# Optimization experiments

Measured on AMD Instinct MI355X. Metric: run time of the kernel, lower is better.

## Reference

```python
import jax, jax.numpy as jnp
import numpy as np

LENGTH_SCALE = 0.1


def setup_inputs() -> dict:
    key = jax.random.key(0)
    k1, k2, k3 = jax.random.split(key, 3)
    features = jax.random.normal(k1, (8, 512, 128, 128), dtype=jnp.float32)
    # nn.Parameter init: normal(0, 0.05)
    weights = jax.random.normal(k2, (16, 64, 512), dtype=jnp.float32) * 0.05
    m = jax.random.normal(k3, (16, 64), dtype=jnp.float32)
    N = jnp.ones((64,), dtype=jnp.float32) * 12.0  # buffer init: ones * 12
    return {"features": features, "weights": weights, "m": m, "N": N}


def reference(features, weights, m, N):
    # per-class linear embedding projection: [b,f,h,w] x [e,c,f] -> [b,e,c,h,w]
    embeddings = jnp.einsum('bfhw,ecf->bechw', features, weights)
    centroids = m / N  # [e, c]
    gamma = -1.0 / (2.0 * LENGTH_SCALE ** 2)
    diff = embeddings - centroids[None, :, :, None, None]
    # squared L2, mean over embedding dim e, RBF exp -> [b, c, h, w]
    out = jnp.exp(jnp.mean(diff * diff, axis=1) * gamma)
    return out
```

## Files before the change

### kernel.cpp

```cpp
#include <hip/hip_runtime.h>

typedef __attribute__((ext_vector_type(8))) short bf16x8;
typedef __attribute__((ext_vector_type(4))) float f32x4;
typedef __attribute__((ext_vector_type(4))) float f4;
typedef __attribute__((ext_vector_type(2))) unsigned int u32x2;
typedef __attribute__((ext_vector_type(4))) unsigned int u32x4;

#define HW   16384
#define FDIM 512

__device__ __forceinline__ unsigned pkhi(float a, float b) {
    return __builtin_amdgcn_perm(__builtin_bit_cast(unsigned int, b),
                                 __builtin_bit_cast(unsigned int, a),
                                 0x07060302u);
}
__device__ __forceinline__ float trhi(float a) {
    return __builtin_bit_cast(float, __builtin_bit_cast(unsigned int, a) & 0xFFFF0000u);
}
__device__ __forceinline__ unsigned pklo(float a, float b) {
    return pkhi(a - trhi(a), b - trhi(b));
}

__global__ __launch_bounds__(256) void duq_fused(
    const float* __restrict__ feat,
    const float* __restrict__ wts,
    const float* __restrict__ m_in,
    const float* __restrict__ n_in,
    float* __restrict__ out)
{
    __shared__ __align__(16) unsigned short Ah[128 * 40];
    __shared__ __align__(16) unsigned short Al[128 * 40];
    __shared__ __align__(16) unsigned short Bh[128 * 40];
    __shared__ __align__(16) unsigned short Bl[128 * 40];

    const int t  = threadIdx.x;
    const int bx = blockIdx.x;
    const int nb = bx & 7;
    const int mb = bx >> 3;
    const int bidx = mb >> 7;
    const int hw0  = (mb & 127) << 7;

    const int fb = t & 7;
    const int pb = t >> 3;
    const float* ap = feat + (size_t)bidx * (FDIM * HW) + (size_t)(fb * 4) * HW + (hw0 + pb * 4);

    const int bn  = t >> 1;
    const int bh_ = t & 1;
    const int ng  = nb * 128 + bn;
    const float* bp = wts + (size_t)((ng & 15) * 64 + (ng >> 4)) * FDIM + bh_ * 16;

    unsigned short* awH = &Ah[(pb * 4) * 40 + fb * 4];
    unsigned short* awL = &Al[(pb * 4) * 40 + fb * 4];
    unsigned short* bwH = &Bh[bn * 40 + bh_ * 16];
    unsigned short* bwL = &Bl[bn * 40 + bh_ * 16];

    const int lane = t & 63;
    const int wv = t >> 6;
    const int wm = wv >> 1, wn = wv & 1;
    const int l16 = lane & 15, qd = lane >> 4;

    const unsigned short* arH = &Ah[(wm * 64 + l16) * 40 + qd * 8];
    const unsigned short* arL = &Al[(wm * 64 + l16) * 40 + qd * 8];
    const unsigned short* brH = &Bh[(wn * 64 + l16) * 40 + qd * 8];
    const unsigned short* brL = &Bl[(wn * 64 + l16) * 40 + qd * 8];

    f32x4 acc[4][4] = {};

    f4 av[4], bv[4];
    #pragma unroll
    for (int i = 0; i < 4; ++i) av[i] = *(const f4*)(ap + (size_t)i * HW);
    #pragma unroll
    for (int q = 0; q < 4; ++q) bv[q] = *(const f4*)(bp + q * 4);

    for (int kt = 0; kt < 16; ++kt) {
        __syncthreads();
        #pragma unroll
        for (int j = 0; j < 4; ++j) {
            float a0 = av[0][j], a1 = av[1][j], a2 = av[2][j], a3 = av[3][j];
            u32x2 h, l;
            h[0] = pkhi(a0, a1); h[1] = pkhi(a2, a3);
            l[0] = pklo(a0, a1); l[1] = pklo(a2, a3);
            *(u32x2*)(awH + j * 40) = h;
            *(u32x2*)(awL + j * 40) = l;
        }
        {
            u32x4 h0 = { pkhi(bv[0][0], bv[0][1]), pkhi(bv[0][2], bv[0][3]),
                         pkhi(bv[1][0], bv[1][1]), pkhi(bv[1][2], bv[1][3]) };
            u32x4 h1 = { pkhi(bv[2][0], bv[2][1]), pkhi(bv[2][2], bv[2][3]),
                         pkhi(bv[3][0], bv[3][1]), pkhi(bv[3][2], bv[3][3]) };
            u32x4 l0 = { pklo(bv[0][0], bv[0][1]), pklo(bv[0][2], bv[0][3]),
                         pklo(bv[1][0], bv[1][1]), pklo(bv[1][2], bv[1][3]) };
            u32x4 l1 = { pklo(bv[2][0], bv[2][1]), pklo(bv[2][2], bv[2][3]),
                         pklo(bv[3][0], bv[3][1]), pklo(bv[3][2], bv[3][3]) };
            *(u32x4*)(bwH)     = h0;  *(u32x4*)(bwH + 8) = h1;
            *(u32x4*)(bwL)     = l0;  *(u32x4*)(bwL + 8) = l1;
        }
        __syncthreads();

        if (kt < 15) {
            ap += 32 * HW;
            bp += 32;
            #pragma unroll
            for (int i = 0; i < 4; ++i) av[i] = *(const f4*)(ap + (size_t)i * HW);
            #pragma unroll
            for (int q = 0; q < 4; ++q) bv[q] = *(const f4*)(bp + q * 4);
        }

        bf16x8 fah[4], fal[4];
        #pragma unroll
        for (int i = 0; i < 4; ++i) {
            fah[i] = *(const bf16x8*)(arH + i * 640);
            fal[i] = *(const bf16x8*)(arL + i * 640);
        }
        #pragma unroll
        for (int j = 0; j < 4; ++j) {
            bf16x8 fbh = *(const bf16x8*)(brH + j * 640);
            bf16x8 fbl = *(const bf16x8*)(brL + j * 640);
            #pragma unroll
            for (int i = 0; i < 4; ++i) {
                acc[i][j] = __builtin_amdgcn_mfma_f32_16x16x32_bf16(fah[i], fbh, acc[i][j], 0, 0, 0);
                acc[i][j] = __builtin_amdgcn_mfma_f32_16x16x32_bf16(fah[i], fbl, acc[i][j], 0, 0, 0);
                acc[i][j] = __builtin_amdgcn_mfma_f32_16x16x32_bf16(fal[i], fbh, acc[i][j], 0, 0, 0);
            }
        }
    }

    float centv[4];
    #pragma unroll
    for (int j = 0; j < 4; ++j) {
        int cj = nb * 8 + wn * 4 + j;
        centv[j] = m_in[l16 * 64 + cj] / n_in[cj];
    }
    #pragma unroll
    for (int i = 0; i < 4; ++i) {
        #pragma unroll
        for (int j = 0; j < 4; ++j) {
            float s0 = acc[i][j][0] - centv[j]; s0 *= s0;
            float s1 = acc[i][j][1] - centv[j]; s1 *= s1;
            float s2 = acc[i][j][2] - centv[j]; s2 *= s2;
            float s3 = acc[i][j][3] - centv[j]; s3 *= s3;
            #pragma unroll
            for (int msk = 1; msk < 16; msk <<= 1) {
                s0 += __shfl_xor(s0, msk, 64);
                s1 += __shfl_xor(s1, msk, 64);
                s2 += __shfl_xor(s2, msk, 64);
                s3 += __shfl_xor(s3, msk, 64);
            }
            if (l16 == 0) {
                int cj = nb * 8 + wn * 4 + j;
                f4 o;
                o[0] = __expf(s0 * -3.125f);
                o[1] = __expf(s1 * -3.125f);
                o[2] = __expf(s2 * -3.125f);
                o[3] = __expf(s3 * -3.125f);
                size_t off = ((size_t)(bidx * 64 + cj)) * HW
                           + (size_t)(hw0 + wm * 64 + i * 16 + qd * 4);
                *(f4*)(out + off) = o;
            }
        }
    }
}

extern "C" void kernel_launch(void* const* d_in, const int* in_sizes, int n_in,
                              void* d_out, int out_size, void* d_ws, size_t ws_size,
                              hipStream_t stream) {
    const float* feat = (const float*)d_in[0];
    const float* wts  = (const float*)d_in[1];
    const float* mbuf = (const float*)d_in[2];
    const float* nbuf = (const float*)d_in[3];
    float* out = (float*)d_out;
    duq_fused<<<dim3(1024 * 8), dim3(256), 0, stream>>>(feat, wts, mbuf, nbuf, out);
}
```

Measured before the change: 754.8 us.

## Precompute bf16 hi/lo weight split in prepass and stream B fragments from global

Adds a small pre-kernel that converts the weights once per call into bf16 hi/lo arrays in workspace, laid out in MFMA fragment order. The main kernel then drops the B shared-memory tiles and per-block weight conversion, loading B fragments straight from global (L2) with one-step register prefetch. It also sets launch_bounds occupancy to 4 blocks. This removes redundant conversion work and LDS traffic, at the cost of an extra launch, more global/L2 loads per wave, and a fallback path when workspace is too small.

```diff
diff --git a/kernel.cpp b/kernel.cpp
--- a/kernel.cpp
+++ b/kernel.cpp
@@ -21,11 +21,147 @@
     return pkhi(a - trhi(a), b - trhi(b));
 }
 
-__global__ __launch_bounds__(256) void duq_fused(
+__global__ __launch_bounds__(256) void conv_w(const float* __restrict__ wts,
+                                              unsigned short* __restrict__ wh,
+                                              unsigned short* __restrict__ wl) {
+    const int tid = blockIdx.x * 256 + threadIdx.x;
+    const int n  = tid & 1023;
+    const int kc = tid >> 10;
+    const float* src = wts + (size_t)((n & 15) * 64 + (n >> 4)) * FDIM + kc * 8;
+    f4 a = *(const f4*)src, b = *(const f4*)(src + 4);
+    u32x4 h = { pkhi(a[0], a[1]), pkhi(a[2], a[3]), pkhi(b[0], b[1]), pkhi(b[2], b[3]) };
+    u32x4 l = { pklo(a[0], a[1]), pklo(a[2], a[3]), pklo(b[0], b[1]), pklo(b[2], b[3]) };
+    size_t off = ((size_t)kc * 1024 + n) * 8;
+    *(u32x4*)(wh + off) = h;
+    *(u32x4*)(wl + off) = l;
+}
+
+__global__ __launch_bounds__(256, 4) void duq_main(
     const float* __restrict__ feat,
-    const float* __restrict__ wts,
+    const unsigned short* __restrict__ wh,
+    const unsigned short* __restrict__ wl,
     const float* __restrict__ m_in,
     const float* __restrict__ n_in,
+    float* __restrict__ out)
+{
+    __shared__ __align__(16) unsigned short Ah[128 * 40];
+    __shared__ __align__(16) unsigned short Al[128 * 40];
+
+    const int t  = threadIdx.x;
+    const int bx = blockIdx.x;
+    const int nb = bx & 7;
+    const int mb = bx >> 3;
+    const int bidx = mb >> 7;
+    const int hw0  = (mb & 127) << 7;
+
+    const int fb = t & 7;
+    const int pb = t >> 3;
+    const float* ap = feat + (size_t)bidx * (FDIM * HW) + (size_t)(fb * 4) * HW + (hw0 + pb * 4);
+    unsigned short* awH = &Ah[(pb * 4) * 40 + fb * 4];
+    unsigned short* awL = &Al[(pb * 4) * 40 + fb * 4];
+
+    const int lane = t & 63;
+    const int wv = t >> 6;
+    const int wm = wv >> 1, wn = wv & 1;
+    const int l16 = lane & 15, qd = lane >> 4;
+
+    const unsigned short* arH = &Ah[(wm * 64 + l16) * 40 + qd * 8];
+    const unsigned short* arL = &Al[(wm * 64 + l16) * 40 + qd * 8];
+
+    const size_t bgoff = ((size_t)qd * 1024 + (size_t)(nb * 128 + wn * 64 + l16)) * 8;
+    const unsigned short* bgh = wh + bgoff;
+    const unsigned short* bgl = wl + bgoff;
+
+    f32x4 acc[4][4] = {};
+
+    f4 av[4];
+    #pragma unroll
+    for (int i = 0; i < 4; ++i) av[i] = *(const f4*)(ap + (size_t)i * HW);
+
+    bf16x8 cbh = *(const bf16x8*)(bgh);
+    bf16x8 cbl = *(const bf16x8*)(bgl);
+    size_t boff = 0;
+
+    for (int kt = 0; kt < 16; ++kt) {
+        __syncthreads();
+        #pragma unroll
+        for (int j = 0; j < 4; ++j) {
+            float a0 = av[0][j], a1 = av[1][j], a2 = av[2][j], a3 = av[3][j];
+            u32x2 h, l;
+            h[0] = pkhi(a0, a1); h[1] = pkhi(a2, a3);
+            l[0] = pklo(a0, a1); l[1] = pklo(a2, a3);
+            *(u32x2*)(awH + j * 40) = h;
+            *(u32x2*)(awL + j * 40) = l;
+        }
+        __syncthreads();
+
+        if (kt < 15) {
+            ap += 32 * HW;
+            #pragma unroll
+            for (int i = 0; i < 4; ++i) av[i] = *(const f4*)(ap + (size_t)i * HW);
+        }
+
+        bf16x8 fah[4], fal[4];
+        #pragma unroll
+        for (int i = 0; i < 4; ++i) {
+            fah[i] = *(const bf16x8*)(arH + i * 640);
+            fal[i] = *(const bf16x8*)(arL + i * 640);
+        }
+
+        #pragma unroll
+        for (int j = 0; j < 4; ++j) {
+            size_t bnext = boff + ((j == 3) ? (size_t)(32768 - 384) : (size_t)128);
+            bf16x8 nbh = *(const bf16x8*)(bgh + bnext);
+            bf16x8 nbl = *(const bf16x8*)(bgl + bnext);
+            #pragma unroll
+            for (int i = 0; i < 4; ++i) {
+                acc[i][j] = __builtin_amdgcn_mfma_f32_16x16x32_bf16(fah[i], cbh, acc[i][j], 0, 0, 0);
+                acc[i][j] = __builtin_amdgcn_mfma_f32_16x16x32_bf16(fah[i], cbl, acc[i][j], 0, 0, 0);
+                acc[i][j] = __builtin_amdgcn_mfma_f32_16x16x32_bf16(fal[i], cbh, acc[i][j], 0, 0, 0);
+            }
+            cbh = nbh; cbl = nbl; boff = bnext;
+        }
+    }
+
+    float centv[4];
+    #pragma unroll
+    for (int j = 0; j < 4; ++j) {
+        int cj = nb * 8 + wn * 4 + j;
+        centv[j] = m_in[l16 * 64 + cj] / n_in[cj];
+    }
+    #pragma unroll
+    for (int i = 0; i < 4; ++i) {
+        #pragma unroll
+        for (int j = 0; j < 4; ++j) {
+            float s0 = acc[i][j][0] - centv[j]; s0 *= s0;
+            float s1 = acc[i][j][1] - centv[j]; s1 *= s1;
+            float s2 = acc[i][j][2] - centv[j]; s2 *= s2;
+            float s3 = acc[i][j][3] - centv[j]; s3 *= s3;
+            #pragma unroll
+            for (int msk = 1; msk < 16; msk <<= 1) {
+                s0 += __shfl_xor(s0, msk, 64);
+                s1 += __shfl_xor(s1, msk, 64);
+                s2 += __shfl_xor(s2, msk, 64);
+                s3 += __shfl_xor(s3, msk, 64);
+            }
+            if (l16 == 0) {
+                int cj = nb * 8 + wn * 4 + j;
+                f4 o;
+                o[0] = __expf(s0 * -3.125f);
+                o[1] = __expf(s1 * -3.125f);
+                o[2] = __expf(s2 * -3.125f);
+                o[3] = __expf(s3 * -3.125f);
+                size_t off = ((size_t)(bidx * 64 + cj)) * HW
+                           + (size_t)(hw0 + wm * 64 + i * 16 + qd * 4);
+                *(f4*)(out + off) = o;
+            }
+        }
+    }
+}
+
+__global__ __launch_bounds__(256) void duq_fallback(
+    const float* __restrict__ feat, const float* __restrict__ wts,
+    const float* __restrict__ m_in, const float* __restrict__ n_in,
     float* __restrict__ out)
 {
     __shared__ __align__(16) unsigned short Ah[128 * 40];
@@ -169,5 +305,13 @@
     const float* mbuf = (const float*)d_in[2];
     const float* nbuf = (const float*)d_in[3];
     float* out = (float*)d_out;
-    duq_fused<<<dim3(1024 * 8), dim3(256), 0, stream>>>(feat, wts, mbuf, nbuf, out);
-}
+
+    if (ws_size >= (size_t)(2 * 1024 * 1024 + 128 * 1024)) {
+        unsigned short* wh = (unsigned short*)d_ws;
+        unsigned short* wl = wh + 512 * 1024;
+        conv_w<<<dim3(256), dim3(256), 0, stream>>>(wts, wh, wl);
+        duq_main<<<dim3(1024 * 8), dim3(256), 0, stream>>>(feat, wh, wl, mbuf, nbuf, out);
+    } else {
+        duq_fallback<<<dim3(1024 * 8), dim3(256), 0, stream>>>(feat, wts, mbuf, nbuf, out);
+    }
+}
```

Result: faster. 726.5 us (-3.7%).
